# Optimization experiments

Hardware: AMD Instinct MI355X
Metric: run time of the kernel (lower is better)

The kernel has to match this reference:

```python
import jax, jax.numpy as jnp
import numpy as np

B, N, D, H = 4, 8192, 1024, 8
HD = D // H  # 128
EPS = 1e-5


def setup_inputs() -> dict:
    key = jax.random.key(0)
    k1, k2, k3 = jax.random.split(key, 3)
    x = jax.random.normal(k1, (B, N, D), dtype=jnp.float32)
    mask = jax.random.randint(k2, (B, 1, N), 0, 2).astype(jnp.bool_)
    # nn.Linear(dim, 3*dim, bias=False): weight [3D, D]; store as [D, 3D] for x @ w
    w_qkv = jax.random.normal(k3, (D, 3 * D), dtype=jnp.float32) / np.sqrt(D)
    gamma = jnp.ones((D,), dtype=jnp.float32)
    beta = jnp.zeros((D,), dtype=jnp.float32)
    return {"x": x, "mask": mask, "w_qkv": w_qkv, "gamma": gamma, "beta": beta}


def _layernorm(x, gamma, beta):
    mu = jnp.mean(x, axis=-1, keepdims=True)
    var = jnp.mean(jnp.square(x - mu), axis=-1, keepdims=True)
    return (x - mu) * jax.lax.rsqrt(var + EPS) * gamma + beta


def reference(x, mask, w_qkv, gamma, beta):
    xn = _layernorm(x, gamma, beta)                       # [B,N,D]
    qkv = xn @ w_qkv                                      # [B,N,3D]
    q, k, v = jnp.split(qkv, 3, axis=-1)
    # 'b n (h d) -> b h n d'
    def to_heads(t):
        return t.reshape(B, N, H, HD).transpose(0, 2, 1, 3)
    q, k, v = to_heads(q), to_heads(k), to_heads(v)       # [B,H,N,HD]
    q = jax.nn.sigmoid(q)
    k = jnp.tanh(k)
    k = jnp.where(mask[..., None], 0.0, k)                # masked_fill -> 0
    kv = jnp.einsum('bhnd,bhne->bhde', k, v)              # k^T @ v, [B,H,HD,HD]
    out = jnp.einsum('bhnd,bhde->bhne', q, kv)            # [B,H,N,HD]
    out = out.transpose(0, 2, 1, 3).reshape(B, N, D)      # 'b h n d -> b n (h d)'
    return out  # output_layer='None' -> Identity
```

## Files before the change

kernel.cpp:

```cpp
#include <hip/hip_runtime.h>

#define EPS 1e-5f
#define B_ 4
#define N_ 8192
#define D_ 1024
#define H_ 8
#define HD_ 128
#define M_TOT 32768
#define NQKV 3072

typedef __bf16 bf16x8 __attribute__((ext_vector_type(8)));
typedef float f32x4 __attribute__((ext_vector_type(4)));

__device__ __forceinline__ float bf2f(unsigned short u) {
    unsigned int v = ((unsigned int)u) << 16;
    return __uint_as_float(v);
}
__device__ __forceinline__ unsigned short f2bf(float f) {
    unsigned int u = __float_as_uint(f);
    u += 0x7fffu + ((u >> 16) & 1u);
    return (unsigned short)(u >> 16);
}

__device__ __forceinline__ float fast_sigmoid(float v) {
    return __builtin_amdgcn_rcpf(1.0f + __expf(-v));
}
__device__ __forceinline__ float fast_tanh(float v) {
    return 1.0f - 2.0f * __builtin_amdgcn_rcpf(1.0f + __expf(2.0f * v));
}

__device__ __forceinline__ void gl_lds16(const void* g, void* l) {
    __builtin_amdgcn_global_load_lds(
        (const __attribute__((address_space(1))) unsigned int*)g,
        (__attribute__((address_space(3))) unsigned int*)l, 16, 0, 0);
}

__global__ __launch_bounds__(256) void ln_kernel(const float* __restrict__ x,
                                                 const float* __restrict__ gamma,
                                                 const float* __restrict__ beta,
                                                 unsigned short* __restrict__ xn) {
    const int row = blockIdx.x;
    const int t = threadIdx.x;
    const float* xr = x + (size_t)row * D_;
    float4 xv = ((const float4*)xr)[t];
    float s = xv.x + xv.y + xv.z + xv.w;
    float s2 = xv.x * xv.x + xv.y * xv.y + xv.z * xv.z + xv.w * xv.w;
    for (int off = 32; off > 0; off >>= 1) {
        s += __shfl_down(s, off);
        s2 += __shfl_down(s2, off);
    }
    __shared__ float red[8];
    if ((t & 63) == 0) { red[t >> 6] = s; red[4 + (t >> 6)] = s2; }
    __syncthreads();
    float ts = red[0] + red[1] + red[2] + red[3];
    float ts2 = red[4] + red[5] + red[6] + red[7];
    float mu = ts * (1.0f / D_);
    float var = ts2 * (1.0f / D_) - mu * mu;
    float rs = rsqrtf(var + EPS);
    float4 g = ((const float4*)gamma)[t];
    float4 bt = ((const float4*)beta)[t];
    ushort4 o;
    o.x = f2bf((xv.x - mu) * rs * g.x + bt.x);
    o.y = f2bf((xv.y - mu) * rs * g.y + bt.y);
    o.z = f2bf((xv.z - mu) * rs * g.z + bt.z);
    o.w = f2bf((xv.w - mu) * rs * g.w + bt.w);
    ((ushort4*)(xn + (size_t)row * D_))[t] = o;
}

__global__ __launch_bounds__(256) void wt_kernel(const float* __restrict__ w,
                                                 unsigned short* __restrict__ wT) {
    __shared__ float tile[64][65];
    const int n0 = blockIdx.x * 64;
    const int k0 = blockIdx.y * 64;
    const int t = threadIdx.x;
    const int tx = t & 63, ty = t >> 6;
    #pragma unroll
    for (int i = 0; i < 16; i++) {
        int r = i * 4 + ty;
        tile[r][tx] = w[(size_t)(k0 + r) * NQKV + n0 + tx];
    }
    __syncthreads();
    #pragma unroll
    for (int i = 0; i < 16; i++) {
        int r = i * 4 + ty;
        wT[(size_t)(n0 + r) * D_ + k0 + tx] = f2bf(tile[tx][r]);
    }
}

#define CT_STRIDE 136
__global__ __launch_bounds__(256, 3) void qkv_gemm(const unsigned short* __restrict__ xn,
                                                   const unsigned short* __restrict__ wT,
                                                   const int* __restrict__ mask,
                                                   unsigned short* __restrict__ qws,
                                                   unsigned short* __restrict__ kT,
                                                   unsigned short* __restrict__ vT) {
    __shared__ unsigned short ShB[128 * CT_STRIDE];
    const int t = threadIdx.x;
    const int w = t >> 6, l = t & 63;
    const int quad = l >> 4, ln16 = l & 15;
    const int m0 = blockIdx.y * 128;
    const int n0 = blockIdx.x * 128;
    const int wm = (w >> 1) * 64, wn = (w & 1) * 64;

    f32x4 acc[4][4] = {};

    const unsigned short* aG = xn + (size_t)(m0 + w * 16 + (l >> 2)) * D_ + (l & 3) * 8;
    const unsigned short* bG = wT + (size_t)(n0 + w * 16 + (l >> 2)) * D_ + (l & 3) * 8;
    char* SB = (char*)ShB;

    for (int k0 = 0; k0 < 1024; k0 += 64) {
        #pragma unroll
        for (int s = 0; s < 2; s++) {
            gl_lds16(aG + k0 + s * 32,            SB + s * 8192 + w * 1024);
            gl_lds16(aG + 64 * D_ + k0 + s * 32,  SB + s * 8192 + 4096 + w * 1024);
            gl_lds16(bG + k0 + s * 32,            SB + 16384 + s * 8192 + w * 1024);
            gl_lds16(bG + 64 * D_ + k0 + s * 32,  SB + 16384 + s * 8192 + 4096 + w * 1024);
        }
        __syncthreads();
        #pragma unroll
        for (int s = 0; s < 2; s++) {
            const char* A0 = SB + s * 8192;
            const char* B0 = SB + 16384 + s * 8192;
            bf16x8 af[4], bfr[4];
            #pragma unroll
            for (int mi = 0; mi < 4; mi++)
                af[mi] = *(const bf16x8*)(A0 + (wm + mi * 16 + ln16) * 64 + quad * 16);
            #pragma unroll
            for (int ni = 0; ni < 4; ni++)
                bfr[ni] = *(const bf16x8*)(B0 + (wn + ni * 16 + ln16) * 64 + quad * 16);
            #pragma unroll
            for (int mi = 0; mi < 4; mi++)
                #pragma unroll
                for (int ni = 0; ni < 4; ni++)
                    acc[mi][ni] = __builtin_amdgcn_mfma_f32_16x16x32_bf16(af[mi], bfr[ni],
                                                                          acc[mi][ni], 0, 0, 0);
        }
        __syncthreads();
    }

    const int region = n0 >> 10;
    const int cbase = n0 & 1023;
    if (region == 0) {
        #pragma unroll
        for (int mi = 0; mi < 4; mi++) {
            #pragma unroll
            for (int r = 0; r < 4; r++) {
                int gm = m0 + wm + mi * 16 + quad * 4 + r;
                #pragma unroll
                for (int ni = 0; ni < 4; ni++) {
                    int cc = cbase + wn + ni * 16 + ln16;
                    qws[(size_t)gm * D_ + cc] = f2bf(fast_sigmoid(acc[mi][ni][r]));
                }
            }
        }
    } else {
        #pragma unroll
        for (int mi = 0; mi < 4; mi++) {
            int tok0 = wm + mi * 16 + quad * 4;
            int mk0 = 0, mk1 = 0, mk2 = 0, mk3 = 0;
            if (region == 1) {
                mk0 = mask[m0 + tok0];
                mk1 = mask[m0 + tok0 + 1];
                mk2 = mask[m0 + tok0 + 2];
                mk3 = mask[m0 + tok0 + 3];
            }
            #pragma unroll
            for (int ni = 0; ni < 4; ni++) {
                int fl = wn + ni * 16 + ln16;
                float v0 = acc[mi][ni][0], v1 = acc[mi][ni][1];
                float v2 = acc[mi][ni][2], v3 = acc[mi][ni][3];
                if (region == 1) {
                    v0 = mk0 ? 0.0f : fast_tanh(v0);
                    v1 = mk1 ? 0.0f : fast_tanh(v1);
                    v2 = mk2 ? 0.0f : fast_tanh(v2);
                    v3 = mk3 ? 0.0f : fast_tanh(v3);
                }
                ushort4 pk;
                pk.x = f2bf(v0); pk.y = f2bf(v1); pk.z = f2bf(v2); pk.w = f2bf(v3);
                *(ushort4*)&ShB[fl * CT_STRIDE + tok0] = pk;
            }
        }
        __syncthreads();
        unsigned short* dstT = (region == 1) ? kT : vT;
        const int h = cbase >> 7;
        const int b = m0 >> 13;
        const int ntok0 = m0 & 8191;
        #pragma unroll
        for (int p = 0; p < 8; p++) {
            int fl = p * 16 + (t >> 4);
            int tok = (t & 15) * 8;
            uint4 u = *(const uint4*)&ShB[fl * CT_STRIDE + tok];
            *(uint4*)(dstT + ((size_t)(b * 8 + h) * 128 + fl) * 8192 + ntok0 + tok) = u;
        }
    }
}

__global__ __launch_bounds__(256) void kv_mfma(const unsigned short* __restrict__ kT,
                                               const unsigned short* __restrict__ vT,
                                               float* __restrict__ kv) {
    __shared__ unsigned short As[128 * 32];
    __shared__ unsigned short Bs[128 * 32];
    const int t = threadIdx.x;
    const int w = t >> 6, l = t & 63;
    const int quad = l >> 4, ln16 = l & 15;
    const int bh = blockIdx.y;
    const int kc0 = blockIdx.x * 512;
    const int wm = (w >> 1) * 64, wn = (w & 1) * 64;

    f32x4 acc[4][4] = {};

    const size_t base = (size_t)bh * 128 * 8192;
    const unsigned short* aG = kT + base + (size_t)(w * 16 + (l >> 2)) * 8192
                               + (l & 3) * 8 + kc0;
    const unsigned short* bG = vT + base + (size_t)(w * 16 + (l >> 2)) * 8192
                               + (l & 3) * 8 + kc0;
    char* AsB = (char*)As;
    char* BsB = (char*)Bs;
    char* aL0 = AsB + w * 1024;
    char* aL1 = AsB + 4096 + w * 1024;
    char* bL0 = BsB + w * 1024;
    char* bL1 = BsB + 4096 + w * 1024;

    for (int kk = 0; kk < 512; kk += 32) {
        gl_lds16(aG + kk, aL0);
        gl_lds16(aG + 64 * 8192 + kk, aL1);
        gl_lds16(bG + kk, bL0);
        gl_lds16(bG + 64 * 8192 + kk, bL1);
        __syncthreads();
        bf16x8 af[4], bfr[4];
        #pragma unroll
        for (int mi = 0; mi < 4; mi++)
            af[mi] = *(const bf16x8*)(AsB + (wm + mi * 16 + ln16) * 64 + quad * 16);
        #pragma unroll
        for (int ni = 0; ni < 4; ni++)
            bfr[ni] = *(const bf16x8*)(BsB + (wn + ni * 16 + ln16) * 64 + quad * 16);
        #pragma unroll
        for (int mi = 0; mi < 4; mi++)
            #pragma unroll
            for (int ni = 0; ni < 4; ni++)
                acc[mi][ni] = __builtin_amdgcn_mfma_f32_16x16x32_bf16(af[mi], bfr[ni],
                                                                      acc[mi][ni], 0, 0, 0);
        __syncthreads();
    }

    float* dst = kv + (size_t)bh * (HD_ * HD_);
    #pragma unroll
    for (int mi = 0; mi < 4; mi++) {
        #pragma unroll
        for (int r = 0; r < 4; r++) {
            int d = wm + mi * 16 + quad * 4 + r;
            #pragma unroll
            for (int ni = 0; ni < 4; ni++) {
                int e = wn + ni * 16 + ln16;
                atomicAdd(&dst[d * HD_ + e], acc[mi][ni][r]);
            }
        }
    }
}

__global__ __launch_bounds__(256) void kvcvt(const float* __restrict__ kv,
                                             unsigned short* __restrict__ kvTb) {
    __shared__ float tile[32][132];
    const int bh = blockIdx.x;
    const int c = blockIdx.y;
    const int t = threadIdx.x;
    {
        int r = t >> 3, cc = (t & 7) * 16;
        const float* src = kv + ((size_t)bh * 128 + c * 32 + r) * 128 + cc;
        #pragma unroll
        for (int q4 = 0; q4 < 4; q4++)
            *(float4*)&tile[r][cc + q4 * 4] = *(const float4*)(src + q4 * 4);
    }
    __syncthreads();
    {
        int e = t >> 1, dh = t & 1;
        ushort4 o[4];
        #pragma unroll
        for (int q4 = 0; q4 < 4; q4++) {
            o[q4].x = f2bf(tile[dh * 16 + q4 * 4 + 0][e]);
            o[q4].y = f2bf(tile[dh * 16 + q4 * 4 + 1][e]);
            o[q4].z = f2bf(tile[dh * 16 + q4 * 4 + 2][e]);
            o[q4].w = f2bf(tile[dh * 16 + q4 * 4 + 3][e]);
        }
        unsigned short* dst = kvTb + (size_t)bh * 16384 + e * 128 + c * 32 + dh * 16;
        #pragma unroll
        for (int q4 = 0; q4 < 4; q4++)
            ((ushort4*)dst)[q4] = o[q4];
    }
}

__global__ __launch_bounds__(256) void out_mfma(const unsigned short* __restrict__ qws,
                                                const unsigned short* __restrict__ kvTb,
                                                float* __restrict__ out) {
    __shared__ unsigned short As[128 * 32];
    __shared__ unsigned short Bs[128 * 32];
    const int t = threadIdx.x;
    const int w = t >> 6, l = t & 63;
    const int quad = l >> 4, ln16 = l & 15;
    const int m0 = blockIdx.x * 128;
    const int h = blockIdx.y;
    const int b = m0 >> 13;
    const int bh = b * 8 + h;
    const int wm = (w >> 1) * 64, wn = (w & 1) * 64;

    f32x4 acc[4][4] = {};

    const unsigned short* aG = qws + (size_t)(m0 + w * 16 + (l >> 2)) * D_
                               + h * HD_ + (l & 3) * 8;
    const unsigned short* bG = kvTb + (size_t)bh * 16384
                               + (size_t)(w * 16 + (l >> 2)) * 128 + (l & 3) * 8;
    char* AsB = (char*)As;
    char* BsB = (char*)Bs;

    for (int kk = 0; kk < 128; kk += 32) {
        gl_lds16(aG + kk, AsB + w * 1024);
        gl_lds16(aG + 64 * D_ + kk, AsB + 4096 + w * 1024);
        gl_lds16(bG + kk, BsB + w * 1024);
        gl_lds16(bG + 64 * 128 + kk, BsB + 4096 + w * 1024);
        __syncthreads();
        bf16x8 af[4], bfr[4];
        #pragma unroll
        for (int mi = 0; mi < 4; mi++)
            af[mi] = *(const bf16x8*)(AsB + (wm + mi * 16 + ln16) * 64 + quad * 16);
        #pragma unroll
        for (int ni = 0; ni < 4; ni++)
            bfr[ni] = *(const bf16x8*)(BsB + (wn + ni * 16 + ln16) * 64 + quad * 16);
        #pragma unroll
        for (int mi = 0; mi < 4; mi++)
            #pragma unroll
            for (int ni = 0; ni < 4; ni++)
                acc[mi][ni] = __builtin_amdgcn_mfma_f32_16x16x32_bf16(af[mi], bfr[ni],
                                                                      acc[mi][ni], 0, 0, 0);
        __syncthreads();
    }

    #pragma unroll
    for (int mi = 0; mi < 4; mi++) {
        #pragma unroll
        for (int r = 0; r < 4; r++) {
            int gm = m0 + wm + mi * 16 + quad * 4 + r;
            #pragma unroll
            for (int ni = 0; ni < 4; ni++) {
                int e = wn + ni * 16 + ln16;
                out[(size_t)gm * D_ + h * HD_ + e] = acc[mi][ni][r];
            }
        }
    }
}

extern "C" void kernel_launch(void* const* d_in, const int* in_sizes, int n_in,
                              void* d_out, int out_size, void* d_ws, size_t ws_size,
                              hipStream_t stream) {
    const float* x     = (const float*)d_in[0];
    const int*   mask  = (const int*)d_in[1];
    const float* w     = (const float*)d_in[2];
    const float* gamma = (const float*)d_in[3];
    const float* beta  = (const float*)d_in[4];
    float* out = (float*)d_out;
    char* ws = (char*)d_ws;

    unsigned short* xn  = (unsigned short*)(ws + 0);
    unsigned short* wT  = (unsigned short*)(ws + 67108864ull);
    unsigned short* qws = (unsigned short*)(ws + 73400320ull);
    unsigned short* kT  = (unsigned short*)(ws + 140509184ull);
    unsigned short* vT  = (unsigned short*)(ws + 207618048ull);
    float* kv           = (float*)(ws + 274726912ull);
    unsigned short* kvTb = (unsigned short*)(ws + 276824064ull);

    hipMemsetAsync(kv, 0, 32 * HD_ * HD_ * sizeof(float), stream);
    hipLaunchKernelGGL(ln_kernel, dim3(M_TOT), dim3(256), 0, stream, x, gamma, beta, xn);
    hipLaunchKernelGGL(wt_kernel, dim3(48, 16), dim3(256), 0, stream, w, wT);
    hipLaunchKernelGGL(qkv_gemm, dim3(NQKV / 128, M_TOT / 128), dim3(256), 0, stream,
                       xn, wT, mask, qws, kT, vT);
    hipLaunchKernelGGL(kv_mfma, dim3(16, 32), dim3(256), 0, stream, kT, vT, kv);
    hipLaunchKernelGGL(kvcvt, dim3(32, 4), dim3(256), 0, stream, kv, kvTb);
    hipLaunchKernelGGL(out_mfma, dim3(M_TOT / 128, 8), dim3(256), 0, stream,
                       qws, kvTb, out);
}
```

Before: 544.6 us.

## Rewrite QKV GEMM with 256x256 tiles, double-buffered LDS and swizzled pipeline

Replaces the 128x128-tile QKV GEMM with a 512-thread, 256x256-tile kernel. It double-buffers LDS staging with explicit vmcnt/lgkmcnt waits and barriers, uses XOR-swizzled LDS layouts to avoid bank conflicts, raises MFMA priority with setprio, and remaps block IDs so tiles are visited in a grouped order for L2 reuse. The transposed K/V epilogue now runs in two passes through shared memory, one per head. This aims to cut global/LDS traffic per FLOP and overlap loads with MFMA, at the cost of 128KB LDS per block, lower occupancy and a fragile hand-written wait schedule.

```diff
diff --git a/kernel.cpp b/kernel.cpp
--- a/kernel.cpp
+++ b/kernel.cpp
@@ -87,113 +87,197 @@
     }
 }
 
-#define CT_STRIDE 136
-__global__ __launch_bounds__(256, 3) void qkv_gemm(const unsigned short* __restrict__ xn,
+
+#define BAR()   asm volatile("s_barrier" ::: "memory")
+#define LGKM0() asm volatile("s_waitcnt lgkmcnt(0)" ::: "memory")
+#define VM4()   asm volatile("s_waitcnt vmcnt(4)" ::: "memory")
+#define VM0()   asm volatile("s_waitcnt vmcnt(0)" ::: "memory")
+
+#define STAGE(dstTile, srcB, h, ktv) do {                                   \
+    const char* s0_ = (srcB) + (size_t)(h) * 262144 + (size_t)(ktv) * 128;  \
+    char* d0_ = (dstTile) + (h) * 16384 + w * 1024;                         \
+    gl_lds16(s0_, d0_);                                                     \
+    gl_lds16(s0_ + 131072, d0_ + 8192);                                     \
+} while (0)
+
+#define LDA(Ab, mhv) do {                                                   \
+    _Pragma("unroll") for (int i_ = 0; i_ < 4; i_++) {                      \
+        const char* rp_ = (Ab) + (size_t)(wm + (mhv) * 64 + i_ * 16 + ln16) * 128; \
+        af[i_][0] = *(const bf16x8*)(rp_ + kc0);                            \
+        af[i_][1] = *(const bf16x8*)(rp_ + kc1);                            \
+    } } while (0)
+
+#define LDB(Bb, nhv) do {                                                   \
+    _Pragma("unroll") for (int j_ = 0; j_ < 2; j_++) {                      \
+        const char* rp_ = (Bb) + (size_t)(wn + (nhv) * 32 + j_ * 16 + ln16) * 128; \
+        bfr[nhv][j_][0] = *(const bf16x8*)(rp_ + kc0);                      \
+        bfr[nhv][j_][1] = *(const bf16x8*)(rp_ + kc1);                      \
+    } } while (0)
+
+#define MFMAQ(mhv, nhv) do {                                                \
+    __builtin_amdgcn_s_setprio(1);                                          \
+    _Pragma("unroll") for (int i_ = 0; i_ < 4; i_++)                        \
+    _Pragma("unroll") for (int j_ = 0; j_ < 2; j_++) {                      \
+        f32x4* ap_ = &acc[(mhv) * 4 + i_][(nhv) * 2 + j_];                  \
+        *ap_ = __builtin_amdgcn_mfma_f32_16x16x32_bf16(af[i_][0], bfr[nhv][j_][0], *ap_, 0, 0, 0); \
+        *ap_ = __builtin_amdgcn_mfma_f32_16x16x32_bf16(af[i_][1], bfr[nhv][j_][1], *ap_, 0, 0, 0); \
+    }                                                                       \
+    __builtin_amdgcn_s_setprio(0);                                          \
+} while (0)
+
+__global__ __launch_bounds__(512, 2) void qkv_gemm(const unsigned short* __restrict__ xn,
                                                    const unsigned short* __restrict__ wT,
                                                    const int* __restrict__ mask,
                                                    unsigned short* __restrict__ qws,
                                                    unsigned short* __restrict__ kT,
                                                    unsigned short* __restrict__ vT) {
-    __shared__ unsigned short ShB[128 * CT_STRIDE];
+    __shared__ __align__(16) char smem[131072];
     const int t = threadIdx.x;
     const int w = t >> 6, l = t & 63;
     const int quad = l >> 4, ln16 = l & 15;
-    const int m0 = blockIdx.y * 128;
-    const int n0 = blockIdx.x * 128;
-    const int wm = (w >> 1) * 64, wn = (w & 1) * 64;
-
-    f32x4 acc[4][4] = {};
-
-    const unsigned short* aG = xn + (size_t)(m0 + w * 16 + (l >> 2)) * D_ + (l & 3) * 8;
-    const unsigned short* bG = wT + (size_t)(n0 + w * 16 + (l >> 2)) * D_ + (l & 3) * 8;
-    char* SB = (char*)ShB;
-
-    for (int k0 = 0; k0 < 1024; k0 += 64) {
-        #pragma unroll
-        for (int s = 0; s < 2; s++) {
-            gl_lds16(aG + k0 + s * 32,            SB + s * 8192 + w * 1024);
-            gl_lds16(aG + 64 * D_ + k0 + s * 32,  SB + s * 8192 + 4096 + w * 1024);
-            gl_lds16(bG + k0 + s * 32,            SB + 16384 + s * 8192 + w * 1024);
-            gl_lds16(bG + 64 * D_ + k0 + s * 32,  SB + 16384 + s * 8192 + 4096 + w * 1024);
-        }
-        __syncthreads();
-        #pragma unroll
-        for (int s = 0; s < 2; s++) {
-            const char* A0 = SB + s * 8192;
-            const char* B0 = SB + 16384 + s * 8192;
-            bf16x8 af[4], bfr[4];
-            #pragma unroll
-            for (int mi = 0; mi < 4; mi++)
-                af[mi] = *(const bf16x8*)(A0 + (wm + mi * 16 + ln16) * 64 + quad * 16);
-            #pragma unroll
-            for (int ni = 0; ni < 4; ni++)
-                bfr[ni] = *(const bf16x8*)(B0 + (wn + ni * 16 + ln16) * 64 + quad * 16);
-            #pragma unroll
-            for (int mi = 0; mi < 4; mi++)
-                #pragma unroll
-                for (int ni = 0; ni < 4; ni++)
-                    acc[mi][ni] = __builtin_amdgcn_mfma_f32_16x16x32_bf16(af[mi], bfr[ni],
-                                                                          acc[mi][ni], 0, 0, 0);
-        }
-        __syncthreads();
+
+    const int lin = blockIdx.x;
+    const int swz = (lin & 7) * 192 + (lin >> 3);
+    const int mt = swz / 12, nt = swz - mt * 12;
+    const int m0 = mt * 256, n0 = nt * 256;
+    const int wm = (w >> 2) * 128, wn = (w & 3) * 64;
+
+    char* Abuf0 = smem;
+    char* Bbuf0 = smem + 32768;
+    char* Abuf1 = smem + 65536;
+    char* Bbuf1 = smem + 98304;
+
+    const int gsw = (l & 7) ^ (l >> 3);
+    const char* aSrc = (const char*)xn + ((size_t)(m0 + w * 8 + (l >> 3)) * 2048) + gsw * 16;
+    const char* bSrc = (const char*)wT + ((size_t)(n0 + w * 8 + (l >> 3)) * 2048) + gsw * 16;
+
+    const int r7 = ln16 & 7;
+    const int kc0 = ((quad ^ r7) << 4);
+    const int kc1 = (((4 | quad) ^ r7) << 4);
+
+    f32x4 acc[8][4] = {};
+    bf16x8 af[4][2];
+    bf16x8 bfr[2][2][2];
+
+    STAGE(Bbuf0, bSrc, 0, 0); STAGE(Abuf0, aSrc, 0, 0);
+    STAGE(Bbuf0, bSrc, 1, 0); STAGE(Abuf0, aSrc, 1, 0);
+    STAGE(Bbuf1, bSrc, 0, 1); STAGE(Abuf1, aSrc, 0, 1);
+    VM4();
+    BAR();
+
+    for (int itn = 0; itn < 8; ++itn) {
+        const int ktHi = 2 * itn + 1;
+        const int kt2 = 2 * itn + 2, kt3 = 2 * itn + 3;
+        const bool pf = (itn < 7);
+
+        LDA(Abuf0, 0); LDB(Bbuf0, 0);
+        STAGE(Bbuf1, bSrc, 1, ktHi);
+        BAR(); LGKM0(); MFMAQ(0, 0); BAR();
+
+        LDB(Bbuf0, 1);
+        STAGE(Abuf1, aSrc, 1, ktHi);
+        BAR(); LGKM0(); MFMAQ(0, 1); BAR();
+
+        LDA(Abuf0, 1);
+        if (pf) STAGE(Bbuf0, bSrc, 0, kt2);
+        BAR(); LGKM0(); MFMAQ(1, 0); BAR();
+
+        if (pf) STAGE(Abuf0, aSrc, 0, kt2);
+        BAR(); MFMAQ(1, 1);
+        if (pf) { VM4(); } else { VM0(); }
+        BAR();
+
+        LDA(Abuf1, 0); LDB(Bbuf1, 0);
+        if (pf) STAGE(Bbuf0, bSrc, 1, kt2);
+        BAR(); LGKM0(); MFMAQ(0, 0); BAR();
+
+        LDB(Bbuf1, 1);
+        if (pf) STAGE(Abuf0, aSrc, 1, kt2);
+        BAR(); LGKM0(); MFMAQ(0, 1); BAR();
+
+        LDA(Abuf1, 1);
+        if (pf) STAGE(Bbuf1, bSrc, 0, kt3);
+        BAR(); LGKM0(); MFMAQ(1, 0); BAR();
+
+        if (pf) STAGE(Abuf1, aSrc, 0, kt3);
+        BAR(); MFMAQ(1, 1);
+        if (pf) { VM4(); }
+        BAR();
     }
 
     const int region = n0 >> 10;
     const int cbase = n0 & 1023;
     if (region == 0) {
         #pragma unroll
-        for (int mi = 0; mi < 4; mi++) {
+        for (int mi = 0; mi < 8; mi++) {
             #pragma unroll
             for (int r = 0; r < 4; r++) {
-                int gm = m0 + wm + mi * 16 + quad * 4 + r;
+                const int gm = m0 + wm + mi * 16 + quad * 4 + r;
+                unsigned short* qr = qws + (size_t)gm * D_ + cbase + wn + ln16;
                 #pragma unroll
-                for (int ni = 0; ni < 4; ni++) {
-                    int cc = cbase + wn + ni * 16 + ln16;
-                    qws[(size_t)gm * D_ + cc] = f2bf(fast_sigmoid(acc[mi][ni][r]));
-                }
+                for (int ni = 0; ni < 4; ni++)
+                    qr[ni * 16] = f2bf(fast_sigmoid(acc[mi][ni][r]));
             }
         }
     } else {
-        #pragma unroll
-        for (int mi = 0; mi < 4; mi++) {
-            int tok0 = wm + mi * 16 + quad * 4;
-            int mk0 = 0, mk1 = 0, mk2 = 0, mk3 = 0;
-            if (region == 1) {
-                mk0 = mask[m0 + tok0];
-                mk1 = mask[m0 + tok0 + 1];
-                mk2 = mask[m0 + tok0 + 2];
-                mk3 = mask[m0 + tok0 + 3];
+        unsigned short* ShT = (unsigned short*)smem;
+        unsigned short* dstT = (region == 1) ? kT : vT;
+        const int bb = m0 >> 13;
+        const int ntok0 = m0 & 8191;
+        const int hbase = cbase >> 7;
+        #pragma unroll
+        for (int pp = 0; pp < 2; pp++) {
+            __syncthreads();
+            if (((wn >> 7) & 1) == pp) {
+                #pragma unroll
+                for (int mi = 0; mi < 8; mi++) {
+                    const int tok0 = wm + mi * 16 + quad * 4;
+                    int mk0 = 0, mk1 = 0, mk2 = 0, mk3 = 0;
+                    if (region == 1) {
+                        mk0 = mask[m0 + tok0];
+                        mk1 = mask[m0 + tok0 + 1];
+                        mk2 = mask[m0 + tok0 + 2];
+                        mk3 = mask[m0 + tok0 + 3];
+                    }
+                    #pragma unroll
+                    for (int ni = 0; ni < 4; ni++) {
+                        const int flp = (wn & 127) + ni * 16 + ln16;
+                        float v0 = acc[mi][ni][0], v1 = acc[mi][ni][1];
+                        float v2 = acc[mi][ni][2], v3 = acc[mi][ni][3];
+                        if (region == 1) {
+                            v0 = mk0 ? 0.0f : fast_tanh(v0);
+                            v1 = mk1 ? 0.0f : fast_tanh(v1);
+                            v2 = mk2 ? 0.0f : fast_tanh(v2);
+                            v3 = mk3 ? 0.0f : fast_tanh(v3);
+                        }
+                        ushort4 pk;
+                        pk.x = f2bf(v0); pk.y = f2bf(v1); pk.z = f2bf(v2); pk.w = f2bf(v3);
+                        *(ushort4*)&ShT[flp * 264 + tok0] = pk;
+                    }
+                }
             }
-            #pragma unroll
-            for (int ni = 0; ni < 4; ni++) {
-                int fl = wn + ni * 16 + ln16;
-                float v0 = acc[mi][ni][0], v1 = acc[mi][ni][1];
-                float v2 = acc[mi][ni][2], v3 = acc[mi][ni][3];
-                if (region == 1) {
-                    v0 = mk0 ? 0.0f : fast_tanh(v0);
-                    v1 = mk1 ? 0.0f : fast_tanh(v1);
-                    v2 = mk2 ? 0.0f : fast_tanh(v2);
-                    v3 = mk3 ? 0.0f : fast_tanh(v3);
-                }
-                ushort4 pk;
-                pk.x = f2bf(v0); pk.y = f2bf(v1); pk.z = f2bf(v2); pk.w = f2bf(v3);
-                *(ushort4*)&ShB[fl * CT_STRIDE + tok0] = pk;
+            __syncthreads();
+            const int h = hbase + pp;
+            unsigned short* dstBase = dstT + ((size_t)(bb * 8 + h) * 128) * 8192 + ntok0;
+            #pragma unroll
+            for (int itc = 0; itc < 8; itc++) {
+                const int idx = itc * 512 + t;
+                const int fl = idx >> 5, ch = idx & 31;
+                uint4 u = *(const uint4*)&ShT[fl * 264 + ch * 8];
+                *(uint4*)(dstBase + (size_t)fl * 8192 + ch * 8) = u;
             }
         }
-        __syncthreads();
-        unsigned short* dstT = (region == 1) ? kT : vT;
-        const int h = cbase >> 7;
-        const int b = m0 >> 13;
-        const int ntok0 = m0 & 8191;
-        #pragma unroll
-        for (int p = 0; p < 8; p++) {
-            int fl = p * 16 + (t >> 4);
-            int tok = (t & 15) * 8;
-            uint4 u = *(const uint4*)&ShB[fl * CT_STRIDE + tok];
-            *(uint4*)(dstT + ((size_t)(b * 8 + h) * 128 + fl) * 8192 + ntok0 + tok) = u;
-        }
-    }
-}
+    }
+}
+
+#undef STAGE
+#undef LDA
+#undef LDB
+#undef MFMAQ
+#undef BAR
+#undef LGKM0
+#undef VM4
+#undef VM0
 
 __global__ __launch_bounds__(256) void kv_mfma(const unsigned short* __restrict__ kT,
                                                const unsigned short* __restrict__ vT,
@@ -370,7 +454,7 @@
     hipMemsetAsync(kv, 0, 32 * HD_ * HD_ * sizeof(float), stream);
     hipLaunchKernelGGL(ln_kernel, dim3(M_TOT), dim3(256), 0, stream, x, gamma, beta, xn);
     hipLaunchKernelGGL(wt_kernel, dim3(48, 16), dim3(256), 0, stream, w, wT);
-    hipLaunchKernelGGL(qkv_gemm, dim3(NQKV / 128, M_TOT / 128), dim3(256), 0, stream,
+    hipLaunchKernelGGL(qkv_gemm, dim3(1536), dim3(512), 0, stream,
                        xn, wT, mask, qws, kT, vT);
     hipLaunchKernelGGL(kv_mfma, dim3(16, 32), dim3(256), 0, stream, kT, vT, kv);
     hipLaunchKernelGGL(kvcvt, dim3(32, 4), dim3(256), 0, stream, kv, kvTb);
```

Result: no change. 553.0 us (+1.5%).
